# Kernel optimization log

Measured on AMD Instinct MI355X. Metric: run time of the kernel, lower is better.

The kernel has to match this reference:

```python
import jax, jax.numpy as jnp
import numpy as np

N = 50000       # num_of_nodes
IN = 256        # in_features
HID = 128       # hidden_features
HEADS = 4       # num_of_heads
E = 800000      # num edges
ALPHA = 0.2     # leaky relu slope
EPS = 1e-6      # layernorm eps
SCALE = float(np.sqrt(HID * HEADS))


def setup_inputs() -> dict:
    key = jax.random.key(0)
    ks = jax.random.split(key, 8)
    data = jax.random.normal(ks[0], (N, IN), dtype=jnp.float32)
    edge = jax.random.randint(ks[1], (2, E), 0, N, dtype=jnp.int64)
    embed_table = jax.random.normal(ks[2], (N, IN), dtype=jnp.float32)
    # per-head Linear(in -> hidden): weight [HEADS, HID, IN], bias [HEADS, HID]
    W = jax.random.normal(ks[3], (HEADS, HID, IN), dtype=jnp.float32) / np.sqrt(IN)
    b = jax.random.normal(ks[4], (HEADS, HID), dtype=jnp.float32) * 0.01
    # attention vectors a: torch.rand -> uniform [0,1)
    a_attn = jax.random.uniform(ks[5], (HEADS, 2 * HID), dtype=jnp.float32)
    ln_gain = jnp.ones((HEADS * HID,), dtype=jnp.float32)
    ln_bias = jnp.zeros((HEADS * HID,), dtype=jnp.float32)
    return {"data": data, "edge": edge, "embed_table": embed_table,
            "W": W, "b": b, "a_attn": a_attn,
            "ln_gain": ln_gain, "ln_bias": ln_bias}


def _leaky(x):
    return jnp.where(x >= 0, x, ALPHA * x)


def reference(data, edge, embed_table, W, b, a_attn, ln_gain, ln_bias):
    # concat=True: input `data` is ignored, nodes come from embedding table
    emb = embed_table.at[0].set(0.0)  # padding_idx=0
    src, dst = edge[0], edge[1]
    heads_out = []
    for h in range(HEADS):  # small fixed head loop
        x = emb @ W[h].T + b[h]                      # [N, HID]
        # score_e = a . [x_src ; x_dst] split into per-node projections
        s1 = x @ a_attn[h, :HID]                     # [N]
        s2 = x @ a_attn[h, HID:]                     # [N]
        e = jnp.exp(_leaky(s1[src] + s2[dst]) / SCALE)   # [E]
        rowsum = jax.ops.segment_sum(e, src, num_segments=N)          # [N]
        agg = jax.ops.segment_sum(e[:, None] * x[dst], src, num_segments=N)  # [N, HID]
        denom = jnp.where(rowsum == 0, 1.0, rowsum)[:, None]
        heads_out.append(agg / denom)
    h_prime = jnp.concatenate(heads_out, axis=1)     # [N, HEADS*HID]
    # LayerNorm with torch unbiased std and (std + eps)
    mean = h_prime.mean(-1, keepdims=True)
    std = jnp.std(h_prime, axis=-1, ddof=1, keepdims=True)
    normed = ln_gain * (h_prime - mean) / (std + EPS) + ln_bias
    return jax.nn.elu(normed)
```

## Files before the change

kernel.cpp:

```cpp
#include <hip/hip_runtime.h>
#include <math.h>

#define N_NODES 50000
#define IN_F    256
#define HID     128
#define HEADS   4
#define NE      800000
#define ALPHA   0.2f
#define LN_EPS  1e-6f
#define OUT_F   512
#define INV_SCALE 0.04419417382415922f
#define STRIDE  96

typedef __attribute__((ext_vector_type(8))) short bf16x8;
typedef __attribute__((ext_vector_type(4))) float f32x4;

static __device__ __forceinline__ unsigned short f2bf(float f) {
  unsigned int u = __float_as_uint(f);
  unsigned int r = (u + 0x7FFFu + ((u >> 16) & 1u)) >> 16;
  return (unsigned short)r;
}
static __device__ __forceinline__ float bf2f(unsigned short h) {
  return __uint_as_float(((unsigned int)h) << 16);
}

__global__ __launch_bounds__(256) void prep_kernel(const float* __restrict__ W,
    unsigned short* __restrict__ WB, int* __restrict__ count)
{
  int i = blockIdx.x * 256 + threadIdx.x;
  float4 v = ((const float4*)W)[i];
  ushort4 o;
  o.x = f2bf(v.x); o.y = f2bf(v.y); o.z = f2bf(v.z); o.w = f2bf(v.w);
  ((ushort4*)WB)[i] = o;
  if (i < N_NODES / 4) ((int4*)count)[i] = make_int4(0, 0, 0, 0);
}

__global__ __launch_bounds__(256, 2) void gemm_fused(
    const float* __restrict__ embF, const unsigned short* __restrict__ WB,
    const float* __restrict__ bias, const float* __restrict__ a_attn,
    unsigned short* __restrict__ X, float* __restrict__ sbuf, int M)
{
  __shared__ unsigned short Wl[32 * 512];
  __shared__ unsigned short Al[4 * 512];
  const int tid = threadIdx.x;
  const int w = tid >> 6, lane = tid & 63;
  const int r = lane & 15, q = lane >> 4;
  const int bm = blockIdx.x * 64;
  f32x4 acc[8][4] = {};
  for (int k0 = 0; k0 < IN_F; k0 += 32) {
    __syncthreads();
    #pragma unroll
    for (int i2 = 0; i2 < 8; ++i2) {
      int c = i2 * 256 + tid;
      int rr = c & 15, qq = (c >> 4) & 3, nt = c >> 6;
      const unsigned short* gp = WB + (size_t)(nt * 16 + rr) * IN_F + k0 + qq * 8;
      __builtin_amdgcn_global_load_lds(
          (const __attribute__((address_space(1))) void*)gp,
          (__attribute__((address_space(3))) void*)(Wl + c * 8), 16, 0, 0);
    }
    {
      int c = tid;
      int rr = c & 15, qq = (c >> 4) & 3, mb = c >> 6;
      int row = min(bm + mb * 16 + rr, M - 1);
      const float* ap = embF + (size_t)row * IN_F + k0 + qq * 8;
      float4 f0 = *(const float4*)ap;
      float4 f1 = *(const float4*)(ap + 4);
      if (row == 0) { f0 = make_float4(0.f,0.f,0.f,0.f); f1 = make_float4(0.f,0.f,0.f,0.f); }
      ushort4 u0 = make_ushort4(f2bf(f0.x), f2bf(f0.y), f2bf(f0.z), f2bf(f0.w));
      ushort4 u1 = make_ushort4(f2bf(f1.x), f2bf(f1.y), f2bf(f1.z), f2bf(f1.w));
      *(ushort4*)(Al + c * 8)     = u0;
      *(ushort4*)(Al + c * 8 + 4) = u1;
    }
    __syncthreads();
    bf16x8 bfrag[4];
    #pragma unroll
    for (int mb = 0; mb < 4; ++mb)
      bfrag[mb] = *(const bf16x8*)(Al + mb * 512 + q * 128 + r * 8);
    #pragma unroll
    for (int t = 0; t < 8; ++t) {
      bf16x8 afrag = *(const bf16x8*)(Wl + (w * 8 + t) * 512 + q * 128 + r * 8);
      #pragma unroll
      for (int mb = 0; mb < 4; ++mb)
        acc[t][mb] = __builtin_amdgcn_mfma_f32_16x16x32_bf16(afrag, bfrag[mb], acc[t][mb], 0, 0, 0);
    }
  }
  const float* a1 = a_attn + w * 2 * HID;
  const float* a2 = a1 + HID;
  #pragma unroll
  for (int mb = 0; mb < 4; ++mb) {
    int m = bm + mb * 16 + r;
    float p1 = 0.f, p2 = 0.f;
    #pragma unroll
    for (int t = 0; t < 8; ++t) {
      int nloc = t * 16 + q * 4;
      int n = w * HID + nloc;
      float4 bz = *(const float4*)(bias + n);
      float x0 = acc[t][mb][0] + bz.x;
      float x1 = acc[t][mb][1] + bz.y;
      float x2 = acc[t][mb][2] + bz.z;
      float x3 = acc[t][mb][3] + bz.w;
      float4 av1 = *(const float4*)(a1 + nloc);
      float4 av2 = *(const float4*)(a2 + nloc);
      p1 += x0 * av1.x + x1 * av1.y + x2 * av1.z + x3 * av1.w;
      p2 += x0 * av2.x + x1 * av2.y + x2 * av2.z + x3 * av2.w;
      if (m < M) {
        ushort4 o = make_ushort4(f2bf(x0), f2bf(x1), f2bf(x2), f2bf(x3));
        *(ushort4*)(X + (size_t)m * OUT_F + n) = o;
      }
    }
    p1 += __shfl_xor(p1, 16, 64); p1 += __shfl_xor(p1, 32, 64);
    p2 += __shfl_xor(p2, 16, 64); p2 += __shfl_xor(p2, 32, 64);
    if (q == 0 && m < M) {
      sbuf[(size_t)m * 8 + w]     = p1;
      sbuf[(size_t)m * 8 + 4 + w] = p2;
    }
  }
}

__global__ void scatter_kernel(const int* __restrict__ src, const int* __restrict__ dst,
                               int* __restrict__ count, unsigned short* __restrict__ rec)
{
  int i = blockIdx.x * blockDim.x + threadIdx.x;
  if (i >= NE) return;
  int s = min(max(src[i], 0), N_NODES - 1);
  int d = min(max(dst[i], 0), N_NODES - 1);
  int slot = atomicAdd(&count[s], 1);
  if (slot < STRIDE) rec[(size_t)s * STRIDE + slot] = (unsigned short)d;
}

__global__ __launch_bounds__(256) void attn_kernel(const unsigned short* __restrict__ X,
    const unsigned short* __restrict__ rec, const int* __restrict__ count,
    const float* __restrict__ sbuf,
    const float* __restrict__ gain, const float* __restrict__ bias,
    float* __restrict__ out)
{
  const int tid = threadIdx.x;
  const int w = tid >> 6, lane = tid & 63;
  const int n = blockIdx.x * 4 + w;
  if (n >= N_NODES) return;
  const int h = lane >> 4;
  const int c0 = lane * 8;
  const unsigned c0b = (unsigned)(c0 * 2);
  const float s1h = sbuf[(size_t)n * 8 + h];
  const int deg = min(count[n], STRIDE);
  const unsigned short* base = rec + (size_t)n * STRIDE;
  const char* Xb = (const char*)X;
  float acc[8] = {};
  float rowsum = 0.f;
  int i = 0;
  for (; i + 8 <= deg; i += 8) {
    uint4 dw = *(const uint4*)(base + i);
    int d0 = dw.x & 0xFFFF, d1 = dw.x >> 16;
    int d2 = dw.y & 0xFFFF, d3 = dw.y >> 16;
    int d4 = dw.z & 0xFFFF, d5 = dw.z >> 16;
    int d6 = dw.w & 0xFFFF, d7 = dw.w >> 16;
    float t0 = s1h + sbuf[(size_t)d0 * 8 + 4 + h];
    float t1 = s1h + sbuf[(size_t)d1 * 8 + 4 + h];
    float t2 = s1h + sbuf[(size_t)d2 * 8 + 4 + h];
    float t3 = s1h + sbuf[(size_t)d3 * 8 + 4 + h];
    float t4 = s1h + sbuf[(size_t)d4 * 8 + 4 + h];
    float t5 = s1h + sbuf[(size_t)d5 * 8 + 4 + h];
    float t6 = s1h + sbuf[(size_t)d6 * 8 + 4 + h];
    float t7 = s1h + sbuf[(size_t)d7 * 8 + 4 + h];
    bf16x8 x0 = *(const bf16x8*)(Xb + (((unsigned)d0 << 10) + c0b));
    bf16x8 x1 = *(const bf16x8*)(Xb + (((unsigned)d1 << 10) + c0b));
    bf16x8 x2 = *(const bf16x8*)(Xb + (((unsigned)d2 << 10) + c0b));
    bf16x8 x3 = *(const bf16x8*)(Xb + (((unsigned)d3 << 10) + c0b));
    bf16x8 x4 = *(const bf16x8*)(Xb + (((unsigned)d4 << 10) + c0b));
    bf16x8 x5 = *(const bf16x8*)(Xb + (((unsigned)d5 << 10) + c0b));
    bf16x8 x6 = *(const bf16x8*)(Xb + (((unsigned)d6 << 10) + c0b));
    bf16x8 x7 = *(const bf16x8*)(Xb + (((unsigned)d7 << 10) + c0b));
    float e0 = __expf((t0 >= 0.f ? t0 : ALPHA * t0) * INV_SCALE);
    float e1 = __expf((t1 >= 0.f ? t1 : ALPHA * t1) * INV_SCALE);
    float e2 = __expf((t2 >= 0.f ? t2 : ALPHA * t2) * INV_SCALE);
    float e3 = __expf((t3 >= 0.f ? t3 : ALPHA * t3) * INV_SCALE);
    float e4 = __expf((t4 >= 0.f ? t4 : ALPHA * t4) * INV_SCALE);
    float e5 = __expf((t5 >= 0.f ? t5 : ALPHA * t5) * INV_SCALE);
    float e6 = __expf((t6 >= 0.f ? t6 : ALPHA * t6) * INV_SCALE);
    float e7 = __expf((t7 >= 0.f ? t7 : ALPHA * t7) * INV_SCALE);
    rowsum += ((e0 + e1) + (e2 + e3)) + ((e4 + e5) + (e6 + e7));
    #pragma unroll
    for (int j = 0; j < 8; ++j) {
      float s = acc[j];
      s += e0 * bf2f((unsigned short)x0[j]);
      s += e1 * bf2f((unsigned short)x1[j]);
      s += e2 * bf2f((unsigned short)x2[j]);
      s += e3 * bf2f((unsigned short)x3[j]);
      s += e4 * bf2f((unsigned short)x4[j]);
      s += e5 * bf2f((unsigned short)x5[j]);
      s += e6 * bf2f((unsigned short)x6[j]);
      s += e7 * bf2f((unsigned short)x7[j]);
      acc[j] = s;
    }
  }
  for (; i < deg; ++i) {
    int d0 = base[i];
    float t0 = s1h + sbuf[(size_t)d0 * 8 + 4 + h];
    bf16x8 x0 = *(const bf16x8*)(Xb + (((unsigned)d0 << 10) + c0b));
    float e0 = __expf((t0 >= 0.f ? t0 : ALPHA * t0) * INV_SCALE);
    rowsum += e0;
    #pragma unroll
    for (int j = 0; j < 8; ++j)
      acc[j] += e0 * bf2f((unsigned short)x0[j]);
  }
  float inv = (rowsum == 0.f) ? 1.f : 1.f / rowsum;
  float v[8];
  float psum = 0.f, psq = 0.f;
  #pragma unroll
  for (int j = 0; j < 8; ++j) {
    v[j] = acc[j] * inv;
    psum += v[j];
    psq  += v[j] * v[j];
  }
  #pragma unroll
  for (int off = 32; off >= 1; off >>= 1) {
    psum += __shfl_xor(psum, off, 64);
    psq  += __shfl_xor(psq,  off, 64);
  }
  float mean = psum * (1.0f / OUT_F);
  float var  = fmaxf((psq - OUT_F * mean * mean) * (1.0f / (OUT_F - 1)), 0.f);
  float inv_std = 1.0f / (sqrtf(var) + LN_EPS);
  float4 g0 = *(const float4*)(gain + c0);
  float4 g1 = *(const float4*)(gain + c0 + 4);
  float4 bb0 = *(const float4*)(bias + c0);
  float4 bb1 = *(const float4*)(bias + c0 + 4);
  float gg[8] = {g0.x, g0.y, g0.z, g0.w, g1.x, g1.y, g1.z, g1.w};
  float bv[8] = {bb0.x, bb0.y, bb0.z, bb0.w, bb1.x, bb1.y, bb1.z, bb1.w};
  float o[8];
  #pragma unroll
  for (int j = 0; j < 8; ++j) {
    float nv = gg[j] * (v[j] - mean) * inv_std + bv[j];
    o[j] = nv > 0.f ? nv : expm1f(nv);
  }
  float* orow = out + (size_t)n * OUT_F + c0;
  *(float4*)(orow)     = make_float4(o[0], o[1], o[2], o[3]);
  *(float4*)(orow + 4) = make_float4(o[4], o[5], o[6], o[7]);
}

extern "C" void kernel_launch(void* const* d_in, const int* in_sizes, int n_in,
                              void* d_out, int out_size, void* d_ws, size_t ws_size,
                              hipStream_t stream)
{
  const int*   edge   = (const int*)d_in[1];
  const float* embed  = (const float*)d_in[2];
  const float* W      = (const float*)d_in[3];
  const float* b      = (const float*)d_in[4];
  const float* a_attn = (const float*)d_in[5];
  const float* ln_g   = (const float*)d_in[6];
  const float* ln_b   = (const float*)d_in[7];
  float* out = (float*)d_out;

  char* ws = (char*)d_ws;
  size_t off = 0;
  auto alloc = [&](size_t bytes) -> void* {
    void* p = ws + off;
    off = (off + bytes + 255) & ~(size_t)255;
    return p;
  };
  unsigned short* WB   = (unsigned short*)alloc((size_t)OUT_F * IN_F * sizeof(unsigned short));
  unsigned short* X    = (unsigned short*)alloc((size_t)N_NODES * OUT_F * sizeof(unsigned short));
  float* sbuf   = (float*)alloc((size_t)N_NODES * 8 * sizeof(float));
  int*   count  = (int*)alloc((size_t)N_NODES * sizeof(int));
  unsigned short* rec = (unsigned short*)alloc((size_t)N_NODES * STRIDE * sizeof(unsigned short));

  const int* src = edge;
  const int* dst = edge + NE;

  prep_kernel<<<(OUT_F * IN_F / 4) / 256, 256, 0, stream>>>(W, WB, count);

  scatter_kernel<<<(NE + 255) / 256, 256, 0, stream>>>(src, dst, count, rec);

  gemm_fused<<<(N_NODES + 63) / 64, 256, 0, stream>>>(embed, WB, b, a_attn, X, sbuf, N_NODES);

  attn_kernel<<<(N_NODES + 3) / 4, 256, 0, stream>>>(X, rec, count, sbuf, ln_g, ln_b, out);
}
```

Baseline: 394.1 us.

## Double-buffer GEMM tiles, retile to 128-row blocks, pad edge counters

The GEMM is rebuilt around 512-thread blocks that each cover 128 rows and half of the output columns. W and embedding tiles are double-buffered in LDS so the next k-slice loads while MFMAs run on the current one, leaving one barrier per step. Each node's edge counter is also padded to its own 64-byte slot, to spread scatter atomics across cache lines and cut contention. The risks are a 16x larger counter array to zero and strided counter reads in the attention kernel, and the embedding rows are now read twice, once per column group.

```diff
diff --git a/kernel.cpp b/kernel.cpp
--- a/kernel.cpp
+++ b/kernel.cpp
@@ -11,6 +11,10 @@
 #define OUT_F   512
 #define INV_SCALE 0.04419417382415922f
 #define STRIDE  96
+#define CPAD    16
+
+#define NBR 391
+#define GEMM_BLOCKS (NBR * 2)
 
 typedef __attribute__((ext_vector_type(8))) short bf16x8;
 typedef __attribute__((ext_vector_type(4))) float f32x4;
@@ -32,75 +36,121 @@
   ushort4 o;
   o.x = f2bf(v.x); o.y = f2bf(v.y); o.z = f2bf(v.z); o.w = f2bf(v.w);
   ((ushort4*)WB)[i] = o;
-  if (i < N_NODES / 4) ((int4*)count)[i] = make_int4(0, 0, 0, 0);
-}
-
-__global__ __launch_bounds__(256, 2) void gemm_fused(
+  for (int j = i; j < N_NODES * CPAD / 4; j += 32768)
+    ((int4*)count)[j] = make_int4(0, 0, 0, 0);
+}
+
+__global__ void scatter_kernel(const int* __restrict__ src, const int* __restrict__ dst,
+                               int* __restrict__ count, unsigned short* __restrict__ rec)
+{
+  int i = blockIdx.x * blockDim.x + threadIdx.x;
+  if (i >= NE) return;
+  int s = min(max(src[i], 0), N_NODES - 1);
+  int d = min(max(dst[i], 0), N_NODES - 1);
+  int slot = atomicAdd(&count[s * CPAD], 1);
+  if (slot < STRIDE) rec[(size_t)s * STRIDE + slot] = (unsigned short)d;
+}
+
+__global__ __launch_bounds__(512, 4) void gemm_fused(
     const float* __restrict__ embF, const unsigned short* __restrict__ WB,
     const float* __restrict__ bias, const float* __restrict__ a_attn,
     unsigned short* __restrict__ X, float* __restrict__ sbuf, int M)
 {
-  __shared__ unsigned short Wl[32 * 512];
-  __shared__ unsigned short Al[4 * 512];
+  __shared__ unsigned short Wl[2][16 * 512];
+  __shared__ unsigned short Al[2][8 * 512];
   const int tid = threadIdx.x;
   const int w = tid >> 6, lane = tid & 63;
   const int r = lane & 15, q = lane >> 4;
-  const int bm = blockIdx.x * 64;
-  f32x4 acc[8][4] = {};
-  for (int k0 = 0; k0 < IN_F; k0 += 32) {
-    __syncthreads();
-    #pragma unroll
-    for (int i2 = 0; i2 < 8; ++i2) {
-      int c = i2 * 256 + tid;
-      int rr = c & 15, qq = (c >> 4) & 3, nt = c >> 6;
-      const unsigned short* gp = WB + (size_t)(nt * 16 + rr) * IN_F + k0 + qq * 8;
-      __builtin_amdgcn_global_load_lds(
-          (const __attribute__((address_space(1))) void*)gp,
-          (__attribute__((address_space(3))) void*)(Wl + c * 8), 16, 0, 0);
-    }
-    {
-      int c = tid;
-      int rr = c & 15, qq = (c >> 4) & 3, mb = c >> 6;
-      int row = min(bm + mb * 16 + rr, M - 1);
-      const float* ap = embF + (size_t)row * IN_F + k0 + qq * 8;
-      float4 f0 = *(const float4*)ap;
-      float4 f1 = *(const float4*)(ap + 4);
-      if (row == 0) { f0 = make_float4(0.f,0.f,0.f,0.f); f1 = make_float4(0.f,0.f,0.f,0.f); }
+  const int rowblk = blockIdx.x >> 1, colgrp = blockIdx.x & 1;
+  const int bm = rowblk * 128;
+  const int cbase = colgrp * 256;
+  const int rc = w & 3, hg = w >> 2;
+  const int head = colgrp * 2 + hg;
+
+  const unsigned short* wg[2];
+  #pragma unroll
+  for (int t2 = 0; t2 < 2; ++t2) {
+    int c = t2 * 512 + tid;
+    int nt = c >> 6, qq = (c >> 4) & 3, rr = c & 15;
+    wg[t2] = WB + (size_t)(cbase + nt * 16 + rr) * IN_F + qq * 8;
+  }
+  const int mbg = tid >> 6, qa = (tid >> 4) & 3, ra = tid & 15;
+  const int arow = min(bm + mbg * 16 + ra, M - 1);
+  const float* ag = embF + (size_t)arow * IN_F + qa * 8;
+  const bool azero = (arow == 0);
+
+  f32x4 acc[8][2] = {};
+  float4 f0, f1;
+
+  #pragma unroll
+  for (int t2 = 0; t2 < 2; ++t2) {
+    int c = t2 * 512 + tid;
+    __builtin_amdgcn_global_load_lds(
+        (const __attribute__((address_space(1))) void*)(wg[t2]),
+        (__attribute__((address_space(3))) void*)(&Wl[0][c * 8]), 16, 0, 0);
+  }
+  f0 = *(const float4*)ag;
+  f1 = *(const float4*)(ag + 4);
+  if (azero) { f0 = make_float4(0.f,0.f,0.f,0.f); f1 = make_float4(0.f,0.f,0.f,0.f); }
+  {
+    ushort4 u0 = make_ushort4(f2bf(f0.x), f2bf(f0.y), f2bf(f0.z), f2bf(f0.w));
+    ushort4 u1 = make_ushort4(f2bf(f1.x), f2bf(f1.y), f2bf(f1.z), f2bf(f1.w));
+    *(ushort4*)(&Al[0][tid * 8])     = u0;
+    *(ushort4*)(&Al[0][tid * 8 + 4]) = u1;
+  }
+  __syncthreads();
+
+  for (int ks = 0; ks < 8; ++ks) {
+    const int cur = ks & 1, nxt = cur ^ 1;
+    const int knext = (ks + 1) * 32;
+    if (ks < 7) {
+      #pragma unroll
+      for (int t2 = 0; t2 < 2; ++t2) {
+        int c = t2 * 512 + tid;
+        __builtin_amdgcn_global_load_lds(
+            (const __attribute__((address_space(1))) void*)(wg[t2] + knext),
+            (__attribute__((address_space(3))) void*)(&Wl[nxt][c * 8]), 16, 0, 0);
+      }
+      f0 = *(const float4*)(ag + knext);
+      f1 = *(const float4*)(ag + knext + 4);
+      if (azero) { f0 = make_float4(0.f,0.f,0.f,0.f); f1 = make_float4(0.f,0.f,0.f,0.f); }
+    }
+    bf16x8 bfrag[2];
+    #pragma unroll
+    for (int mb = 0; mb < 2; ++mb)
+      bfrag[mb] = *(const bf16x8*)(&Al[cur][(rc * 2 + mb) * 512 + q * 128 + r * 8]);
+    #pragma unroll
+    for (int t = 0; t < 8; ++t) {
+      bf16x8 afrag = *(const bf16x8*)(&Wl[cur][(hg * 8 + t) * 512 + q * 128 + r * 8]);
+      acc[t][0] = __builtin_amdgcn_mfma_f32_16x16x32_bf16(afrag, bfrag[0], acc[t][0], 0, 0, 0);
+      acc[t][1] = __builtin_amdgcn_mfma_f32_16x16x32_bf16(afrag, bfrag[1], acc[t][1], 0, 0, 0);
+    }
+    if (ks < 7) {
       ushort4 u0 = make_ushort4(f2bf(f0.x), f2bf(f0.y), f2bf(f0.z), f2bf(f0.w));
       ushort4 u1 = make_ushort4(f2bf(f1.x), f2bf(f1.y), f2bf(f1.z), f2bf(f1.w));
-      *(ushort4*)(Al + c * 8)     = u0;
-      *(ushort4*)(Al + c * 8 + 4) = u1;
+      *(ushort4*)(&Al[nxt][tid * 8])     = u0;
+      *(ushort4*)(&Al[nxt][tid * 8 + 4]) = u1;
     }
     __syncthreads();
-    bf16x8 bfrag[4];
-    #pragma unroll
-    for (int mb = 0; mb < 4; ++mb)
-      bfrag[mb] = *(const bf16x8*)(Al + mb * 512 + q * 128 + r * 8);
+  }
+
+  const float* a1 = a_attn + head * 2 * HID;
+  const float* a2 = a1 + HID;
+  #pragma unroll
+  for (int mb = 0; mb < 2; ++mb) {
+    int m = bm + rc * 32 + mb * 16 + r;
+    float p1 = 0.f, p2 = 0.f;
     #pragma unroll
     for (int t = 0; t < 8; ++t) {
-      bf16x8 afrag = *(const bf16x8*)(Wl + (w * 8 + t) * 512 + q * 128 + r * 8);
-      #pragma unroll
-      for (int mb = 0; mb < 4; ++mb)
-        acc[t][mb] = __builtin_amdgcn_mfma_f32_16x16x32_bf16(afrag, bfrag[mb], acc[t][mb], 0, 0, 0);
-    }
-  }
-  const float* a1 = a_attn + w * 2 * HID;
-  const float* a2 = a1 + HID;
-  #pragma unroll
-  for (int mb = 0; mb < 4; ++mb) {
-    int m = bm + mb * 16 + r;
-    float p1 = 0.f, p2 = 0.f;
-    #pragma unroll
-    for (int t = 0; t < 8; ++t) {
-      int nloc = t * 16 + q * 4;
-      int n = w * HID + nloc;
+      int nl = t * 16 + q * 4;
+      int n = head * HID + nl;
       float4 bz = *(const float4*)(bias + n);
       float x0 = acc[t][mb][0] + bz.x;
       float x1 = acc[t][mb][1] + bz.y;
       float x2 = acc[t][mb][2] + bz.z;
       float x3 = acc[t][mb][3] + bz.w;
-      float4 av1 = *(const float4*)(a1 + nloc);
-      float4 av2 = *(const float4*)(a2 + nloc);
+      float4 av1 = *(const float4*)(a1 + nl);
+      float4 av2 = *(const float4*)(a2 + nl);
       p1 += x0 * av1.x + x1 * av1.y + x2 * av1.z + x3 * av1.w;
       p2 += x0 * av2.x + x1 * av2.y + x2 * av2.z + x3 * av2.w;
       if (m < M) {
@@ -111,21 +161,10 @@
     p1 += __shfl_xor(p1, 16, 64); p1 += __shfl_xor(p1, 32, 64);
     p2 += __shfl_xor(p2, 16, 64); p2 += __shfl_xor(p2, 32, 64);
     if (q == 0 && m < M) {
-      sbuf[(size_t)m * 8 + w]     = p1;
-      sbuf[(size_t)m * 8 + 4 + w] = p2;
-    }
-  }
-}
-
-__global__ void scatter_kernel(const int* __restrict__ src, const int* __restrict__ dst,
-                               int* __restrict__ count, unsigned short* __restrict__ rec)
-{
-  int i = blockIdx.x * blockDim.x + threadIdx.x;
-  if (i >= NE) return;
-  int s = min(max(src[i], 0), N_NODES - 1);
-  int d = min(max(dst[i], 0), N_NODES - 1);
-  int slot = atomicAdd(&count[s], 1);
-  if (slot < STRIDE) rec[(size_t)s * STRIDE + slot] = (unsigned short)d;
+      sbuf[(size_t)m * 8 + head]     = p1;
+      sbuf[(size_t)m * 8 + 4 + head] = p2;
+    }
+  }
 }
 
 __global__ __launch_bounds__(256) void attn_kernel(const unsigned short* __restrict__ X,
@@ -142,7 +181,7 @@
   const int c0 = lane * 8;
   const unsigned c0b = (unsigned)(c0 * 2);
   const float s1h = sbuf[(size_t)n * 8 + h];
-  const int deg = min(count[n], STRIDE);
+  const int deg = min(count[n * CPAD], STRIDE);
   const unsigned short* base = rec + (size_t)n * STRIDE;
   const char* Xb = (const char*)X;
   float acc[8] = {};
@@ -260,7 +299,7 @@
   unsigned short* WB   = (unsigned short*)alloc((size_t)OUT_F * IN_F * sizeof(unsigned short));
   unsigned short* X    = (unsigned short*)alloc((size_t)N_NODES * OUT_F * sizeof(unsigned short));
   float* sbuf   = (float*)alloc((size_t)N_NODES * 8 * sizeof(float));
-  int*   count  = (int*)alloc((size_t)N_NODES * sizeof(int));
+  int*   count  = (int*)alloc((size_t)N_NODES * CPAD * sizeof(int));
   unsigned short* rec = (unsigned short*)alloc((size_t)N_NODES * STRIDE * sizeof(unsigned short));
 
   const int* src = edge;
@@ -270,7 +309,7 @@
 
   scatter_kernel<<<(NE + 255) / 256, 256, 0, stream>>>(src, dst, count, rec);
 
-  gemm_fused<<<(N_NODES + 63) / 64, 256, 0, stream>>>(embed, WB, b, a_attn, X, sbuf, N_NODES);
+  gemm_fused<<<GEMM_BLOCKS, 512, 0, stream>>>(embed, WB, b, a_attn, X, sbuf, N_NODES);
 
   attn_kernel<<<(N_NODES + 3) / 4, 256, 0, stream>>>(X, rec, count, sbuf, ln_g, ln_b, out);
 }
```

After: 421.4 us. 6.9% more time.
